# Performance work log

Hardware: AMD Instinct MI355X
Metric: run time of the kernel (lower is better)

The kernel has to match this reference:

```python
import jax, jax.numpy as jnp
import numpy as np

N_HEADS = 64
N_KV_HEADS = 8
HEAD_DIM = 128
HIDDEN = 8192
SEQ = 2048


def setup_inputs() -> dict:
    key = jax.random.key(0)
    k1, k2, k3, k4 = jax.random.split(key, 4)
    scale = 1.0 / np.sqrt(HIDDEN)
    x = jax.random.normal(k1, (1, 1, SEQ, HIDDEN), dtype=jnp.float32)
    wq = jax.random.normal(k2, (HIDDEN, N_HEADS * HEAD_DIM), dtype=jnp.float32) * scale
    wk = jax.random.normal(k3, (HIDDEN, N_KV_HEADS * HEAD_DIM), dtype=jnp.float32) * scale
    wv = jax.random.normal(k4, (HIDDEN, N_KV_HEADS * HEAD_DIM), dtype=jnp.float32) * scale
    return {"x": x, "wq": wq, "wk": wk, "wv": wv}


def reference(x, wq, wk, wv):
    # Fused QKV projection: concat weights along output dim, single matmul.
    qkv_w = jnp.concatenate([wq, wk, wv], axis=-1)  # [H, (64+8+8)*128]
    fused = jnp.einsum('bush,hd->busd', x, qkv_w)    # [1,1,S,10240]
    b, _, s, _ = fused.shape
    q_dim = N_HEADS * HEAD_DIM
    kv_dim = N_KV_HEADS * HEAD_DIM
    q = fused[..., :q_dim]
    k = fused[..., q_dim:q_dim + kv_dim]
    v = fused[..., q_dim + kv_dim:]
    # nlp_create_qkv_heads: [B,1,S,nh*hd] -> [B,nh,S,hd]
    q_heads = q.reshape(b, s, N_HEADS, HEAD_DIM).transpose(0, 2, 1, 3)
    k_heads = k.reshape(b, s, N_KV_HEADS, HEAD_DIM).transpose(0, 2, 1, 3)
    v_heads = v.reshape(b, s, N_KV_HEADS, HEAD_DIM).transpose(0, 2, 1, 3)
    return (q_heads, k_heads, v_heads)
```

## Files before the change

kernel.cpp:

```cpp
#include <hip/hip_runtime.h>
#include <stdint.h>

#define M_DIM 2048
#define K_DIM 8192
#define N_Q   8192
#define N_KV  1024
#define N_TOT (N_Q + 2 * N_KV)

typedef __bf16 bf16x8 __attribute__((ext_vector_type(8)));
typedef __bf16 bf16x2 __attribute__((ext_vector_type(2)));
typedef float  f32x4  __attribute__((ext_vector_type(4)));

__global__ __launch_bounds__(256) void xcast(const float* __restrict__ x,
                                             __bf16* __restrict__ xb) {
    size_t i = ((size_t)blockIdx.x * 256 + threadIdx.x) * 8;
    f32x4 a = *(const f32x4*)(x + i);
    f32x4 b = *(const f32x4*)(x + i + 4);
    bf16x8 o = { (__bf16)a.x, (__bf16)a.y, (__bf16)a.z, (__bf16)a.w,
                 (__bf16)b.x, (__bf16)b.y, (__bf16)b.z, (__bf16)b.w };
    *(bf16x8*)(xb + i) = o;
}

__global__ __launch_bounds__(256) void wcast_t(const float* __restrict__ wq,
                                               const float* __restrict__ wk,
                                               const float* __restrict__ wv,
                                               __bf16* __restrict__ wt) {
    __shared__ float sT[64 * 65];
    const uint32_t bid   = blockIdx.x;
    const uint32_t ktile = bid & 127;
    const uint32_t ntile = bid >> 7;
    const float* W; uint32_t ldW, csrc, cdst;
    if (ntile < 128)      { W = wq; ldW = N_Q;  csrc = ntile * 64;
                            cdst = csrc; }
    else if (ntile < 144) { W = wk; ldW = N_KV; csrc = (ntile - 128) * 64;
                            cdst = N_Q + csrc; }
    else                  { W = wv; ldW = N_KV; csrc = (ntile - 144) * 64;
                            cdst = N_Q + N_KV + csrc; }
    const uint32_t k0 = ktile * 64;
    const uint32_t t  = threadIdx.x;

    const uint32_t lr = t >> 4;
    const uint32_t lc = (t & 15) * 4;
    const float* gp = W + (size_t)(k0 + lr) * ldW + csrc + lc;
    #pragma unroll
    for (int i = 0; i < 4; ++i) {
        f32x4 v = *(const f32x4*)(gp + (size_t)i * 16 * ldW);
        float* d = &sT[(lr + i * 16) * 65 + lc];
        d[0] = v.x; d[1] = v.y; d[2] = v.z; d[3] = v.w;
    }
    __syncthreads();

    const uint32_t wn  = t >> 3;
    const uint32_t wk8 = (t & 7) * 8;
    #pragma unroll
    for (int it = 0; it < 2; ++it) {
        uint32_t n = wn + it * 32;
        bf16x8 o;
        #pragma unroll
        for (int j = 0; j < 8; ++j) o[j] = (__bf16)sT[(wk8 + j) * 65 + n];
        *(bf16x8*)(wt + (size_t)(cdst + n) * K_DIM + k0 + wk8) = o;
    }
}

__device__ __forceinline__ void gload16(const void* g, void* l) {
    __builtin_amdgcn_global_load_lds(
        (const __attribute__((address_space(1))) void*)g,
        (__attribute__((address_space(3))) void*)l, 16, 0, 0);
}

__device__ __forceinline__ uint32_t swz4(uint32_t r) { return (r ^ (r >> 2)) & 3u; }

#define AOFFe(b,h) (((b)*2+(h))*8192)
#define BOFFe(b,h) (32768 + ((b)*2+(h))*8192)

template<int BUF, int MH, int KH, bool LOADB, bool DOWAIT, bool SISA, int SB, int SH>
__device__ __forceinline__ void phase8(uint32_t kk, __bf16* S,
    f32x4 (&acc)[8][4], bf16x8 (&bfr)[4],
    const uint32_t (&aoff)[2][4], const uint32_t (&boff)[4],
    const __bf16* gA0, const __bf16* gA1,
    const __bf16* gB0, const __bf16* gB1, uint32_t w)
{
    if (DOWAIT) asm volatile("s_waitcnt vmcnt(6)" ::: "memory");
    bf16x8 af[4];
    #pragma unroll
    for (int m = 0; m < 4; ++m)
        af[m] = *(const bf16x8*)&S[AOFFe(BUF, KH) + aoff[MH][m]];
    if (LOADB) {
        #pragma unroll
        for (int n = 0; n < 4; ++n)
            bfr[n] = *(const bf16x8*)&S[BOFFe(BUF, KH) + boff[n]];
    }
    {
        const __bf16* g0 = SISA ? gA0 : gB0;
        const __bf16* g1 = SISA ? gA1 : gB1;
        const uint32_t d = (SISA ? AOFFe(SB, SH) : BOFFe(SB, SH)) + w * 512;
        gload16(g0 + kk, &S[d]);
        gload16(g1 + kk, &S[d + 4096]);
    }
    asm volatile("" ::: "memory");
    __builtin_amdgcn_s_barrier();
    asm volatile("" ::: "memory");
    __builtin_amdgcn_s_setprio(1);
    #pragma unroll
    for (int mf = 0; mf < 4; ++mf)
        #pragma unroll
        for (int nf = 0; nf < 4; ++nf)
            acc[MH * 4 + mf][nf] = __builtin_amdgcn_mfma_f32_16x16x32_bf16(
                af[mf], bfr[nf], acc[MH * 4 + mf][nf], 0, 0, 0);
    __builtin_amdgcn_s_setprio(0);
    asm volatile("" ::: "memory");
    __builtin_amdgcn_s_barrier();
    asm volatile("" ::: "memory");
}

#define PSTAGE(ISA, B, H, KK) do {                                        \
    const __bf16* g0_ = (ISA) ? gA0 : gB0;                                \
    const __bf16* g1_ = (ISA) ? gA1 : gB1;                                \
    const uint32_t d_ = ((ISA) ? AOFFe(B, H) : BOFFe(B, H)) + w * 512;    \
    gload16(g0_ + (KK), &S[d_]);                                          \
    gload16(g1_ + (KK), &S[d_ + 4096]);                                   \
} while (0)

__global__ __launch_bounds__(512) void qkv_mm8(const __bf16* __restrict__ xb,
                                               const __bf16* __restrict__ wt,
                                               float* __restrict__ out)
{
    __shared__ __align__(16) __bf16 S[65536];
    const uint32_t tid  = threadIdx.x;
    const uint32_t w    = tid >> 6;
    const uint32_t lane = tid & 63;
    const uint32_t l15  = lane & 15;
    const uint32_t quad = lane >> 4;
    const uint32_t wid_m = w >> 2;
    const uint32_t wid_n = w & 3;

    const uint32_t logical = (blockIdx.x & 7) * 40 + (blockIdx.x >> 3);
    const uint32_t mt = logical & 7;
    const uint32_t nt = logical >> 3;
    const uint32_t m0 = mt * 256;
    const uint32_t n0 = nt * 256;

    const uint32_t lr0 = tid >> 2;
    const uint32_t lr1 = 128 + lr0;
    const uint32_t pos = tid & 3;
    const __bf16* gA0 = xb + (size_t)(m0 + lr0) * K_DIM + (pos ^ swz4(lr0)) * 8;
    const __bf16* gA1 = xb + (size_t)(m0 + lr1) * K_DIM + (pos ^ swz4(lr1)) * 8;
    const __bf16* gB0 = wt + (size_t)(n0 + lr0) * K_DIM + (pos ^ swz4(lr0)) * 8;
    const __bf16* gB1 = wt + (size_t)(n0 + lr1) * K_DIM + (pos ^ swz4(lr1)) * 8;

    uint32_t aoff[2][4], boff[4];
    #pragma unroll
    for (int mh = 0; mh < 2; ++mh)
        #pragma unroll
        for (int m = 0; m < 4; ++m) {
            uint32_t ar = wid_m * 128 + mh * 64 + m * 16 + l15;
            aoff[mh][m] = ar * 32 + (quad ^ swz4(ar)) * 8;
        }
    #pragma unroll
    for (int n = 0; n < 4; ++n) {
        uint32_t br = wid_n * 64 + n * 16 + l15;
        boff[n] = br * 32 + (quad ^ swz4(br)) * 8;
    }

    f32x4 acc[8][4] = {};
    bf16x8 bfr[4];

    PSTAGE(true,  0, 0, 0);
    PSTAGE(false, 0, 0, 0);
    PSTAGE(true,  0, 1, 32);
    PSTAGE(false, 0, 1, 32);
    PSTAGE(true,  1, 0, 64);
    PSTAGE(false, 1, 0, 64);
    asm volatile("s_waitcnt vmcnt(8)" ::: "memory");
    __builtin_amdgcn_s_barrier();
    asm volatile("" ::: "memory");

    for (uint32_t i = 0; i < K_DIM / 128; ++i) {
        const uint32_t kb = i * 128;
        phase8<0,0,0,true ,false, true ,1,1>((kb +  96) & 8191, S, acc, bfr, aoff, boff, gA0, gA1, gB0, gB1, w);
        phase8<0,1,0,false,true , false,1,1>((kb +  96) & 8191, S, acc, bfr, aoff, boff, gA0, gA1, gB0, gB1, w);
        phase8<0,0,1,true ,false, true ,0,0>((kb + 128) & 8191, S, acc, bfr, aoff, boff, gA0, gA1, gB0, gB1, w);
        phase8<0,1,1,false,true , false,0,0>((kb + 128) & 8191, S, acc, bfr, aoff, boff, gA0, gA1, gB0, gB1, w);
        phase8<1,0,0,true ,false, true ,0,1>((kb + 160) & 8191, S, acc, bfr, aoff, boff, gA0, gA1, gB0, gB1, w);
        phase8<1,1,0,false,true , false,0,1>((kb + 160) & 8191, S, acc, bfr, aoff, boff, gA0, gA1, gB0, gB1, w);
        phase8<1,0,1,true ,false, true ,1,0>((kb + 192) & 8191, S, acc, bfr, aoff, boff, gA0, gA1, gB0, gB1, w);
        phase8<1,1,1,false,true , false,1,0>((kb + 192) & 8191, S, acc, bfr, aoff, boff, gA0, gA1, gB0, gB1, w);
    }
    asm volatile("s_waitcnt vmcnt(0)" ::: "memory");

    float* op = out + (size_t)(2 * nt + (wid_n >> 1)) * ((size_t)M_DIM * 128)
                    + (size_t)(m0 + wid_m * 128) * 128 + (wid_n & 1) * 64;
    #pragma unroll
    for (int mi = 0; mi < 8; ++mi)
        #pragma unroll
        for (int rr = 0; rr < 4; ++rr) {
            uint32_t row = mi * 16 + quad * 4 + rr;
            #pragma unroll
            for (int nf = 0; nf < 4; ++nf)
                op[(size_t)row * 128 + nf * 16 + l15] = acc[mi][nf][rr];
        }
}

#define BM 128
#define BN 128
#define BK 32
#define NIT (K_DIM / BK)

__device__ __forceinline__ uint32_t swz_fb(uint32_t r) { return ((r >> 1) ^ (r >> 3)) & 3u; }

__device__ __forceinline__ uint32_t pack_bf16(float lo, float hi) {
    bf16x2 v = { (__bf16)lo, (__bf16)hi };
    return __builtin_bit_cast(uint32_t, v);
}

__global__ __launch_bounds__(256) void qkv_gemm(
    const float* __restrict__ x,
    const float* __restrict__ wq,
    const float* __restrict__ wk,
    const float* __restrict__ wv,
    float* __restrict__ out)
{
    __shared__ __align__(16) uint16_t sA[BM * BK];
    __shared__ __align__(16) uint16_t sB[BN * BK];
    uint32_t* sAu = (uint32_t*)sA;
    uint32_t* sBu = (uint32_t*)sB;

    const uint32_t tid    = threadIdx.x;
    const uint32_t bid    = blockIdx.x;
    const uint32_t mt_blk = bid & 15;
    const uint32_t nt_blk = bid >> 4;
    const uint32_t m0     = mt_blk * BM;

    const size_t QSZ = (size_t)64 * M_DIM * 128;
    const size_t KSZ = (size_t)8  * M_DIM * 128;
    const float* Wsel;
    uint32_t ldW, col0;
    size_t obase;
    if (nt_blk < 64)      { Wsel = wq; ldW = N_Q;  col0 = nt_blk * 128;
                            obase = (size_t)nt_blk * M_DIM * 128; }
    else if (nt_blk < 72) { Wsel = wk; ldW = N_KV; col0 = (nt_blk - 64) * 128;
                            obase = QSZ + (size_t)(nt_blk - 64) * M_DIM * 128; }
    else                  { Wsel = wv; ldW = N_KV; col0 = (nt_blk - 72) * 128;
                            obase = QSZ + KSZ + (size_t)(nt_blk - 72) * M_DIM * 128; }

    const float* agp = x + (size_t)(m0 + (tid >> 3)) * K_DIM + (tid & 7) * 4;
    uint32_t a_wr[4];
    #pragma unroll
    for (int i = 0; i < 4; ++i) {
        uint32_t r = i * 32 + (tid >> 3);
        a_wr[i] = r * 16 + ((((tid >> 1) & 3) ^ swz_fb(r)) * 4) + (tid & 1) * 2;
    }

    const uint32_t bk  = (tid >> 4) * 2;
    const uint32_t bn0 = (tid & 15) * 8;
    const float* bgp = Wsel + (size_t)bk * ldW + col0 + bn0;
    const uint32_t bkc = bk >> 3;
    const uint32_t bkd = (bk & 7) >> 1;

    f32x4 apre[4], bpre[4];
    #pragma unroll
    for (int i = 0; i < 4; ++i) apre[i] = *(const f32x4*)(agp + (size_t)i * 32 * K_DIM);
    bpre[0] = *(const f32x4*)(bgp);
    bpre[1] = *(const f32x4*)(bgp + 4);
    bpre[2] = *(const f32x4*)(bgp + ldW);
    bpre[3] = *(const f32x4*)(bgp + ldW + 4);

    const uint32_t lane = tid & 63;
    const uint32_t wid  = tid >> 6;
    const uint32_t wm   = (wid >> 1) * 64;
    const uint32_t wn   = (wid & 1) * 64;
    const uint32_t l15  = lane & 15;
    const uint32_t quad = lane >> 4;

    f32x4 acc[4][4] = {};

    uint32_t a_off[4], b_off[4];
    #pragma unroll
    for (int t = 0; t < 4; ++t) {
        uint32_t ar = wm + t * 16 + l15;
        a_off[t] = ar * BK + ((quad ^ swz_fb(ar)) * 8);
        uint32_t br = wn + t * 16 + l15;
        b_off[t] = br * BK + ((quad ^ swz_fb(br)) * 8);
    }

    const float* agp_n = agp + BK;
    const float* bgp_n = bgp + (size_t)BK * ldW;

    for (uint32_t kt = 0; kt < NIT; ++kt) {
        __syncthreads();

        #pragma unroll
        for (int i = 0; i < 4; ++i) {
            uint2 wv2;
            wv2.x = pack_bf16(apre[i].x, apre[i].y);
            wv2.y = pack_bf16(apre[i].z, apre[i].w);
            *(uint2*)&sAu[a_wr[i]] = wv2;
        }
        {
            const float* pk0 = (const float*)&bpre[0];
            const float* pk1 = (const float*)&bpre[2];
            #pragma unroll
            for (int j = 0; j < 8; ++j) {
                uint32_t n = bn0 + j;
                sBu[n * 16 + ((bkc ^ swz_fb(n)) * 4) + bkd] = pack_bf16(pk0[j], pk1[j]);
            }
        }

        if (kt + 1 < NIT) {
            #pragma unroll
            for (int i = 0; i < 4; ++i) apre[i] = *(const f32x4*)(agp_n + (size_t)i * 32 * K_DIM);
            bpre[0] = *(const f32x4*)(bgp_n);
            bpre[1] = *(const f32x4*)(bgp_n + 4);
            bpre[2] = *(const f32x4*)(bgp_n + ldW);
            bpre[3] = *(const f32x4*)(bgp_n + ldW + 4);
            agp_n += BK;
            bgp_n += (size_t)BK * ldW;
        }

        __syncthreads();

        bf16x8 af[4], bf[4];
        #pragma unroll
        for (int t = 0; t < 4; ++t) {
            af[t] = *(const bf16x8*)(sA + a_off[t]);
            bf[t] = *(const bf16x8*)(sB + b_off[t]);
        }
        #pragma unroll
        for (int mi = 0; mi < 4; ++mi)
            #pragma unroll
            for (int ni = 0; ni < 4; ++ni)
                acc[mi][ni] = __builtin_amdgcn_mfma_f32_16x16x32_bf16(
                    af[mi], bf[ni], acc[mi][ni], 0, 0, 0);
    }

    float* op = out + obase + (size_t)m0 * 128;
    #pragma unroll
    for (int mi = 0; mi < 4; ++mi) {
        #pragma unroll
        for (int r = 0; r < 4; ++r) {
            uint32_t row = wm + mi * 16 + quad * 4 + r;
            #pragma unroll
            for (int ni = 0; ni < 4; ++ni) {
                uint32_t col = wn + ni * 16 + l15;
                op[(size_t)row * 128 + col] = acc[mi][ni][r];
            }
        }
    }
}

extern "C" void kernel_launch(void* const* d_in, const int* in_sizes, int n_in,
                              void* d_out, int out_size, void* d_ws, size_t ws_size,
                              hipStream_t stream) {
    const float* x  = (const float*)d_in[0];
    const float* wq = (const float*)d_in[1];
    const float* wk = (const float*)d_in[2];
    const float* wv = (const float*)d_in[3];

    const size_t XB_BYTES = (size_t)M_DIM * K_DIM * 2;
    const size_t WT_BYTES = (size_t)N_TOT * K_DIM * 2;

    if (ws_size >= XB_BYTES + WT_BYTES) {
        __bf16* xb = (__bf16*)d_ws;
        __bf16* wt = (__bf16*)((char*)d_ws + XB_BYTES);
        xcast<<<dim3((M_DIM * K_DIM) / (256 * 8)), dim3(256), 0, stream>>>(x, xb);
        wcast_t<<<dim3((K_DIM / 64) * (N_TOT / 64)), dim3(256), 0, stream>>>(wq, wk, wv, wt);
        qkv_mm8<<<dim3((M_DIM / 256) * (N_TOT / 256)), dim3(512), 0, stream>>>(xb, wt, (float*)d_out);
    } else {
        qkv_gemm<<<dim3((M_DIM / BM) * (N_TOT / BN)), dim3(256), 0, stream>>>(
            x, wq, wk, wv, (float*)d_out);
    }
}
```

Measured before the change: 944.6 us.

## Enlarge GEMM N tile to 320 so grid fills exactly one wave

Changes the bf16 MFMA GEMM tile from 256x256 to 256x320, giving each wave 5 N-fragments. The grid now has 256 blocks instead of 320, removing the partial second wave on the device's CUs. The extra 64 B rows are staged with 4-byte global-to-LDS loads, LDS use and the wait counts are reworked, and the epilogue is rewritten per column fragment. In exchange it adds register pressure, small inefficient loads, and drops the block-index swizzle.

```diff
diff --git a/kernel.cpp b/kernel.cpp
--- a/kernel.cpp
+++ b/kernel.cpp
@@ -67,36 +67,32 @@
         (const __attribute__((address_space(1))) void*)g,
         (__attribute__((address_space(3))) void*)l, 16, 0, 0);
 }
+__device__ __forceinline__ void gload4(const void* g, void* l) {
+    __builtin_amdgcn_global_load_lds(
+        (const __attribute__((address_space(1))) void*)g,
+        (__attribute__((address_space(3))) void*)l, 4, 0, 0);
+}
 
 __device__ __forceinline__ uint32_t swz4(uint32_t r) { return (r ^ (r >> 2)) & 3u; }
 
-#define AOFFe(b,h) (((b)*2+(h))*8192)
-#define BOFFe(b,h) (32768 + ((b)*2+(h))*8192)
-
-template<int BUF, int MH, int KH, bool LOADB, bool DOWAIT, bool SISA, int SB, int SH>
-__device__ __forceinline__ void phase8(uint32_t kk, __bf16* S,
-    f32x4 (&acc)[8][4], bf16x8 (&bfr)[4],
-    const uint32_t (&aoff)[2][4], const uint32_t (&boff)[4],
-    const __bf16* gA0, const __bf16* gA1,
-    const __bf16* gB0, const __bf16* gB1, uint32_t w)
+template<int BUF, int MH, int KH, bool LOADB, bool DOWAIT, class F>
+__device__ __forceinline__ void phase5(__bf16* S, f32x4 (&acc)[8][5],
+    bf16x8 (&bfr)[5], const uint32_t (&aoff)[2][4], const uint32_t (&boff)[5],
+    F&& stage)
 {
-    if (DOWAIT) asm volatile("s_waitcnt vmcnt(6)" ::: "memory");
+    if constexpr (DOWAIT) {
+        asm volatile("s_waitcnt vmcnt(9)" ::: "memory");
+    }
     bf16x8 af[4];
     #pragma unroll
     for (int m = 0; m < 4; ++m)
-        af[m] = *(const bf16x8*)&S[AOFFe(BUF, KH) + aoff[MH][m]];
-    if (LOADB) {
-        #pragma unroll
-        for (int n = 0; n < 4; ++n)
-            bfr[n] = *(const bf16x8*)&S[BOFFe(BUF, KH) + boff[n]];
-    }
-    {
-        const __bf16* g0 = SISA ? gA0 : gB0;
-        const __bf16* g1 = SISA ? gA1 : gB1;
-        const uint32_t d = (SISA ? AOFFe(SB, SH) : BOFFe(SB, SH)) + w * 512;
-        gload16(g0 + kk, &S[d]);
-        gload16(g1 + kk, &S[d + 4096]);
-    }
+        af[m] = *(const bf16x8*)&S[(BUF * 2 + KH) * 8192 + aoff[MH][m]];
+    if constexpr (LOADB) {
+        #pragma unroll
+        for (int n = 0; n < 5; ++n)
+            bfr[n] = *(const bf16x8*)&S[32768 + (BUF * 2 + KH) * 10240 + boff[n]];
+    }
+    stage();
     asm volatile("" ::: "memory");
     __builtin_amdgcn_s_barrier();
     asm volatile("" ::: "memory");
@@ -104,7 +100,7 @@
     #pragma unroll
     for (int mf = 0; mf < 4; ++mf)
         #pragma unroll
-        for (int nf = 0; nf < 4; ++nf)
+        for (int nf = 0; nf < 5; ++nf)
             acc[MH * 4 + mf][nf] = __builtin_amdgcn_mfma_f32_16x16x32_bf16(
                 af[mf], bfr[nf], acc[MH * 4 + mf][nf], 0, 0, 0);
     __builtin_amdgcn_s_setprio(0);
@@ -113,19 +109,15 @@
     asm volatile("" ::: "memory");
 }
 
-#define PSTAGE(ISA, B, H, KK) do {                                        \
-    const __bf16* g0_ = (ISA) ? gA0 : gB0;                                \
-    const __bf16* g1_ = (ISA) ? gA1 : gB1;                                \
-    const uint32_t d_ = ((ISA) ? AOFFe(B, H) : BOFFe(B, H)) + w * 512;    \
-    gload16(g0_ + (KK), &S[d_]);                                          \
-    gload16(g1_ + (KK), &S[d_ + 4096]);                                   \
-} while (0)
-
-__global__ __launch_bounds__(512) void qkv_mm8(const __bf16* __restrict__ xb,
+#define STA(b,h,j,kk)  gload16(srcA[j] + (kk), &S[((b)*2+(h))*8192  + (j)*4096 + w512])
+#define STB(b,h,j,kk)  gload16(srcB[j] + (kk), &S[32768 + ((b)*2+(h))*10240 + (j)*4096 + w512])
+#define STB4(b,h,q,kk) gload4 (srcB4[q] + (kk), &S[32768 + ((b)*2+(h))*10240 + 8192 + (q)*1024 + w128])
+
+__global__ __launch_bounds__(512) void qkv_mm5(const __bf16* __restrict__ xb,
                                                const __bf16* __restrict__ wt,
                                                float* __restrict__ out)
 {
-    __shared__ __align__(16) __bf16 S[65536];
+    __shared__ __align__(16) __bf16 S[73728];
     const uint32_t tid  = threadIdx.x;
     const uint32_t w    = tid >> 6;
     const uint32_t lane = tid & 63;
@@ -133,22 +125,32 @@
     const uint32_t quad = lane >> 4;
     const uint32_t wid_m = w >> 2;
     const uint32_t wid_n = w & 3;
-
-    const uint32_t logical = (blockIdx.x & 7) * 40 + (blockIdx.x >> 3);
-    const uint32_t mt = logical & 7;
-    const uint32_t nt = logical >> 3;
+    const uint32_t w512 = w * 512;
+    const uint32_t w128 = w * 128;
+
+    const uint32_t mt = blockIdx.x & 7;
+    const uint32_t nt = blockIdx.x >> 3;
     const uint32_t m0 = mt * 256;
-    const uint32_t n0 = nt * 256;
-
-    const uint32_t lr0 = tid >> 2;
-    const uint32_t lr1 = 128 + lr0;
-    const uint32_t pos = tid & 3;
-    const __bf16* gA0 = xb + (size_t)(m0 + lr0) * K_DIM + (pos ^ swz4(lr0)) * 8;
-    const __bf16* gA1 = xb + (size_t)(m0 + lr1) * K_DIM + (pos ^ swz4(lr1)) * 8;
-    const __bf16* gB0 = wt + (size_t)(n0 + lr0) * K_DIM + (pos ^ swz4(lr0)) * 8;
-    const __bf16* gB1 = wt + (size_t)(n0 + lr1) * K_DIM + (pos ^ swz4(lr1)) * 8;
-
-    uint32_t aoff[2][4], boff[4];
+    const uint32_t n0 = nt * 320;
+
+    const __bf16* srcA[2];
+    const __bf16* srcB[2];
+    const __bf16* srcB4[2];
+    #pragma unroll
+    for (int j = 0; j < 2; ++j) {
+        uint32_t r = j * 128 + (tid >> 2);
+        uint32_t c = (tid & 3) ^ swz4(r);
+        srcA[j] = xb + (size_t)(m0 + r) * K_DIM + c * 8;
+        srcB[j] = wt + (size_t)(n0 + r) * K_DIM + c * 8;
+    }
+    #pragma unroll
+    for (int q = 0; q < 2; ++q) {
+        uint32_t r = 256 + q * 32 + (tid >> 4);
+        uint32_t c = ((tid & 15) >> 2) ^ swz4(r);
+        srcB4[q] = wt + (size_t)(n0 + r) * K_DIM + c * 8 + (tid & 3) * 2;
+    }
+
+    uint32_t aoff[2][4], boff[5];
     #pragma unroll
     for (int mh = 0; mh < 2; ++mh)
         #pragma unroll
@@ -157,48 +159,59 @@
             aoff[mh][m] = ar * 32 + (quad ^ swz4(ar)) * 8;
         }
     #pragma unroll
-    for (int n = 0; n < 4; ++n) {
-        uint32_t br = wid_n * 64 + n * 16 + l15;
+    for (int n = 0; n < 5; ++n) {
+        uint32_t br = wid_n * 80 + n * 16 + l15;
         boff[n] = br * 32 + (quad ^ swz4(br)) * 8;
     }
 
-    f32x4 acc[8][4] = {};
-    bf16x8 bfr[4];
-
-    PSTAGE(true,  0, 0, 0);
-    PSTAGE(false, 0, 0, 0);
-    PSTAGE(true,  0, 1, 32);
-    PSTAGE(false, 0, 1, 32);
-    PSTAGE(true,  1, 0, 64);
-    PSTAGE(false, 1, 0, 64);
-    asm volatile("s_waitcnt vmcnt(8)" ::: "memory");
+    f32x4 acc[8][5] = {};
+    bf16x8 bfr[5];
+
+    STA(0,0,0,0);  STA(0,0,1,0);  STB(0,0,0,0);  STB(0,0,1,0);  STB4(0,0,0,0);  STB4(0,0,1,0);
+    STA(0,1,0,32); STA(0,1,1,32); STB(0,1,0,32); STB(0,1,1,32); STB4(0,1,0,32); STB4(0,1,1,32);
+    STA(1,0,0,64); STA(1,0,1,64); STB(1,0,0,64); STB(1,0,1,64); STB4(1,0,0,64); STB4(1,0,1,64);
+    asm volatile("s_waitcnt vmcnt(12)" ::: "memory");
     __builtin_amdgcn_s_barrier();
     asm volatile("" ::: "memory");
 
     for (uint32_t i = 0; i < K_DIM / 128; ++i) {
         const uint32_t kb = i * 128;
-        phase8<0,0,0,true ,false, true ,1,1>((kb +  96) & 8191, S, acc, bfr, aoff, boff, gA0, gA1, gB0, gB1, w);
-        phase8<0,1,0,false,true , false,1,1>((kb +  96) & 8191, S, acc, bfr, aoff, boff, gA0, gA1, gB0, gB1, w);
-        phase8<0,0,1,true ,false, true ,0,0>((kb + 128) & 8191, S, acc, bfr, aoff, boff, gA0, gA1, gB0, gB1, w);
-        phase8<0,1,1,false,true , false,0,0>((kb + 128) & 8191, S, acc, bfr, aoff, boff, gA0, gA1, gB0, gB1, w);
-        phase8<1,0,0,true ,false, true ,0,1>((kb + 160) & 8191, S, acc, bfr, aoff, boff, gA0, gA1, gB0, gB1, w);
-        phase8<1,1,0,false,true , false,0,1>((kb + 160) & 8191, S, acc, bfr, aoff, boff, gA0, gA1, gB0, gB1, w);
-        phase8<1,0,1,true ,false, true ,1,0>((kb + 192) & 8191, S, acc, bfr, aoff, boff, gA0, gA1, gB0, gB1, w);
-        phase8<1,1,1,false,true , false,1,0>((kb + 192) & 8191, S, acc, bfr, aoff, boff, gA0, gA1, gB0, gB1, w);
+        const uint32_t k0 = kb + 96;
+        const uint32_t k1 = (kb + 128) & 8191;
+        const uint32_t k2 = (kb + 160) & 8191;
+        const uint32_t k3 = (kb + 192) & 8191;
+        phase5<0,0,0,true ,false>(S, acc, bfr, aoff, boff, [&]{
+            STA(1,1,0,k0); STA(1,1,1,k0); STB(1,1,0,k0); });
+        phase5<0,1,0,false,true >(S, acc, bfr, aoff, boff, [&]{
+            STB(1,1,1,k0); STB4(1,1,0,k0); STB4(1,1,1,k0); });
+        phase5<0,0,1,true ,false>(S, acc, bfr, aoff, boff, [&]{
+            STA(0,0,0,k1); STA(0,0,1,k1); STB(0,0,0,k1); });
+        phase5<0,1,1,false,true >(S, acc, bfr, aoff, boff, [&]{
+            STB(0,0,1,k1); STB4(0,0,0,k1); STB4(0,0,1,k1); });
+        phase5<1,0,0,true ,false>(S, acc, bfr, aoff, boff, [&]{
+            STA(0,1,0,k2); STA(0,1,1,k2); STB(0,1,0,k2); });
+        phase5<1,1,0,false,true >(S, acc, bfr, aoff, boff, [&]{
+            STB(0,1,1,k2); STB4(0,1,0,k2); STB4(0,1,1,k2); });
+        phase5<1,0,1,true ,false>(S, acc, bfr, aoff, boff, [&]{
+            STA(1,0,0,k3); STA(1,0,1,k3); STB(1,0,0,k3); });
+        phase5<1,1,1,false,true >(S, acc, bfr, aoff, boff, [&]{
+            STB(1,0,1,k3); STB4(1,0,0,k3); STB4(1,0,1,k3); });
     }
     asm volatile("s_waitcnt vmcnt(0)" ::: "memory");
 
-    float* op = out + (size_t)(2 * nt + (wid_n >> 1)) * ((size_t)M_DIM * 128)
-                    + (size_t)(m0 + wid_m * 128) * 128 + (wid_n & 1) * 64;
-    #pragma unroll
-    for (int mi = 0; mi < 8; ++mi)
-        #pragma unroll
-        for (int rr = 0; rr < 4; ++rr) {
-            uint32_t row = mi * 16 + quad * 4 + rr;
-            #pragma unroll
-            for (int nf = 0; nf < 4; ++nf)
-                op[(size_t)row * 128 + nf * 16 + l15] = acc[mi][nf][rr];
-        }
+    const uint32_t cbase = n0 + wid_n * 80;
+    #pragma unroll
+    for (int nf = 0; nf < 5; ++nf) {
+        const uint32_t c = cbase + nf * 16;
+        float* oph = out + (size_t)(c >> 7) * ((size_t)M_DIM * 128) + (c & 127) + l15;
+        #pragma unroll
+        for (int mi = 0; mi < 8; ++mi)
+            #pragma unroll
+            for (int rr = 0; rr < 4; ++rr) {
+                uint32_t row = m0 + wid_m * 128 + mi * 16 + quad * 4 + rr;
+                oph[(size_t)row * 128] = acc[mi][nf][rr];
+            }
+    }
 }
 
 #define BM 128
@@ -364,7 +377,7 @@
         __bf16* wt = (__bf16*)((char*)d_ws + XB_BYTES);
         xcast<<<dim3((M_DIM * K_DIM) / (256 * 8)), dim3(256), 0, stream>>>(x, xb);
         wcast_t<<<dim3((K_DIM / 64) * (N_TOT / 64)), dim3(256), 0, stream>>>(wq, wk, wv, wt);
-        qkv_mm8<<<dim3((M_DIM / 256) * (N_TOT / 256)), dim3(512), 0, stream>>>(xb, wt, (float*)d_out);
+        qkv_mm5<<<dim3((M_DIM / 256) * (N_TOT / 320)), dim3(512), 0, stream>>>(xb, wt, (float*)d_out);
     } else {
         qkv_gemm<<<dim3((M_DIM / BM) * (N_TOT / BN)), dim3(256), 0, stream>>>(
             x, wq, wk, wv, (float*)d_out);
```

New measurement: 886.2 us. 1.07x faster.
